# Kernel optimization log

Measured on AMD Instinct MI355X. Metric: run time of the kernel, lower is better.

Reference implementation:

```python
import jax, jax.numpy as jnp
import numpy as np

N = 100000
E = 640000
D = 128
L = 3
B = 128
OUT = 10


def setup_inputs() -> dict:
    key = jax.random.key(0)
    ks = jax.random.split(key, 8)
    x = jax.random.normal(ks[0], (N, D), dtype=jnp.float32)
    edge_index = jax.random.randint(ks[1], (2, E), 0, N, dtype=jnp.int64)
    batch = jnp.sort(jax.random.randint(ks[2], (N,), 0, B, dtype=jnp.int64))
    # per-layer GCNConv weights (in==hidden==D so they stack) and biases
    Ws = jax.random.normal(ks[3], (L, D, D), dtype=jnp.float32) / np.sqrt(D)
    bs = jnp.zeros((L, D), dtype=jnp.float32)
    # MLP head: single Linear(hidden -> out), norm=None
    W_mlp = jax.random.normal(ks[4], (D, OUT), dtype=jnp.float32) / np.sqrt(D)
    b_mlp = jnp.zeros((OUT,), dtype=jnp.float32)
    return {"x": x, "edge_index": edge_index, "batch": batch,
            "Ws": Ws, "bs": bs, "W_mlp": W_mlp, "b_mlp": b_mlp}


def reference(x, edge_index, batch, Ws, bs, W_mlp, b_mlp):
    n = x.shape[0]
    # --- GCN normalization (PyG gcn_norm with self-loops, edge_weight=1) ---
    loop = jnp.arange(n, dtype=edge_index.dtype)
    src = jnp.concatenate([edge_index[0], loop])  # message sources (x_j)
    dst = jnp.concatenate([edge_index[1], loop])  # aggregation targets
    deg = jax.ops.segment_sum(jnp.ones_like(dst, dtype=x.dtype), dst, num_segments=n)
    dinv = jnp.where(deg > 0, jax.lax.rsqrt(jnp.maximum(deg, 1.0)), 0.0)
    norm = dinv[src] * dinv[dst]  # [E+N]

    def gcn_conv(h, W, b):
        hw = h @ W  # [N, D] dense transform
        msg = hw[src] * norm[:, None]  # gather + scale [E+N, D]
        agg = jax.ops.segment_sum(msg, dst, num_segments=n)  # scatter-add
        return agg + b

    h = x
    for l in range(Ws.shape[0]):
        h = jax.nn.relu(gcn_conv(h, Ws[l], bs[l]))

    # global add pool over graphs
    pooled = jax.ops.segment_sum(h, batch, num_segments=B)  # [B, D]
    # MLP head (single linear, no norm/act)
    return pooled @ W_mlp + b_mlp
```

## Files before the change

### kernel.cpp

```cpp
#include <hip/hip_runtime.h>
#include <hip/hip_bf16.h>

#define N_NODES 100000
#define N_EDGES 640000
#define DIM 128
#define N_LAYERS 3
#define N_GRAPHS 128
#define N_OUT 10
#define SCAN_BLK 1024
#define N_SCAN_BLKS ((N_NODES + SCAN_BLK - 1) / SCAN_BLK)
#define PCHUNK 128
#define NXCD 8
#define RNODES (N_NODES / NXCD)
#define R_EST 98304
#define BE 1000
#define RK 40
#define GEMM_GRID 512

typedef _Float16 h4 __attribute__((ext_vector_type(4)));
typedef _Float16 h2 __attribute__((ext_vector_type(2)));
typedef _Float16 h8 __attribute__((ext_vector_type(8)));
typedef float f32x4 __attribute__((ext_vector_type(4)));


__global__ __launch_bounds__(256) void bucket_edges(const int* __restrict__ ei,
                                                    int* __restrict__ rangeCur,
                                                    int2* __restrict__ staging) {
    __shared__ int hist[NXCD];
    __shared__ int base[NXCD];
    const int e0 = blockIdx.x * BE;
    if (threadIdx.x < NXCD) hist[threadIdx.x] = 0;
    __syncthreads();

    int s[4], d[4], r[4];
    #pragma unroll
    for (int k = 0; k < 4; ++k) {
        int e = e0 + threadIdx.x + k * 256;
        if (e < e0 + BE) {
            s[k] = ei[e];
            d[k] = ei[N_EDGES + e];
            r[k] = d[k] / RNODES;
            atomicAdd(&hist[r[k]], 1);
        } else r[k] = -1;
    }
    __syncthreads();
    if (threadIdx.x < NXCD) base[threadIdx.x] = atomicAdd(&rangeCur[threadIdx.x], hist[threadIdx.x]);
    __syncthreads();
    if (threadIdx.x < NXCD) hist[threadIdx.x] = 0;
    __syncthreads();

    #pragma unroll
    for (int k = 0; k < 4; ++k) {
        if (r[k] >= 0) {
            int idx = base[r[k]] + atomicAdd(&hist[r[k]], 1);
            staging[(size_t)r[k] * R_EST + idx] = make_int2(s[k], d[k]);
        }
    }
}


__global__ __launch_bounds__(256) void hist_pinned(const int2* __restrict__ staging,
                                                   const int* __restrict__ rangeCur,
                                                   int* __restrict__ cnt) {
    const int g = blockIdx.x & (NXCD - 1);
    const int b = blockIdx.x >> 3;
    const int n = rangeCur[g];
    const int2* st = staging + (size_t)g * R_EST;
    for (int j = b * 256 + threadIdx.x; j < n; j += RK * 256)
        atomicAdd(&cnt[st[j].y], 1);
}


__global__ void scan1(const int* __restrict__ cnt, int* __restrict__ off, int* __restrict__ bsum,
                      float* __restrict__ dinv) {
    __shared__ int tmp[256];
    int base = blockIdx.x * SCAN_BLK + threadIdx.x * 4;
    int c[4];
    #pragma unroll
    for (int k = 0; k < 4; ++k) c[k] = (base + k < N_NODES) ? cnt[base + k] : 0;
    #pragma unroll
    for (int k = 0; k < 4; ++k)
        if (base + k < N_NODES) dinv[base + k] = rsqrtf((float)(c[k] + 1));
    int tot = c[0] + c[1] + c[2] + c[3];
    tmp[threadIdx.x] = tot;
    __syncthreads();
    int val = tot;
    for (int d = 1; d < 256; d <<= 1) {
        int add = (threadIdx.x >= d) ? tmp[threadIdx.x - d] : 0;
        __syncthreads();
        val += add;
        tmp[threadIdx.x] = val;
        __syncthreads();
    }
    int ex = val - tot;
    int e1 = ex + c[0], e2 = e1 + c[1], e3 = e2 + c[2];
    if (base + 0 < N_NODES) off[base + 0] = ex;
    if (base + 1 < N_NODES) off[base + 1] = e1;
    if (base + 2 < N_NODES) off[base + 2] = e2;
    if (base + 3 < N_NODES) off[base + 3] = e3;
    if (threadIdx.x == 255) bsum[blockIdx.x] = val;
}

__global__ void scan2(int* __restrict__ bsum) {
    __shared__ int tmp[128];
    int t = threadIdx.x;
    int v = (t < N_SCAN_BLKS) ? bsum[t] : 0;
    int own = v;
    tmp[t] = v;
    __syncthreads();
    for (int d = 1; d < 128; d <<= 1) {
        int add = (t >= d) ? tmp[t - d] : 0;
        __syncthreads();
        v += add;
        tmp[t] = v;
        __syncthreads();
    }
    if (t < N_SCAN_BLKS) bsum[t] = v - own;
}

__global__ void scan3(int* __restrict__ off, const int* __restrict__ bsum) {
    int i = blockIdx.x * blockDim.x + threadIdx.x;
    if (i < N_NODES) off[i] += bsum[i / SCAN_BLK];
    if (i == 0) off[N_NODES] = N_EDGES;
}


__global__ __launch_bounds__(256) void fill_pinned(const int2* __restrict__ staging,
                                                   const int* __restrict__ rangeCur,
                                                   const int* __restrict__ off,
                                                   int* __restrict__ cursor,
                                                   int* __restrict__ csr_src) {
    const int g = blockIdx.x & (NXCD - 1);
    const int b = blockIdx.x >> 3;
    const int n = rangeCur[g];
    const int2* st = staging + (size_t)g * R_EST;
    for (int j = b * 256 + threadIdx.x; j < n; j += RK * 256) {
        int2 sd = st[j];
        int pos = off[sd.y] + atomicAdd(&cursor[sd.y], 1);
        csr_src[pos] = sd.x;
    }
}


__global__ void wt_prep(const float* __restrict__ Ws, _Float16* __restrict__ wt) {
    int t = blockIdx.x * blockDim.x + threadIdx.x;
    if (t >= N_LAYERS * DIM * 32) return;
    int u = t & 31;
    int n = (t >> 5) & 127;
    int l = t >> 12;
    const float* W = Ws + (size_t)l * DIM * DIM;
    int k0 = u * 4;
    h4 v;
    v.x = (_Float16)W[(k0 + 0) * DIM + n];
    v.y = (_Float16)W[(k0 + 1) * DIM + n];
    v.z = (_Float16)W[(k0 + 2) * DIM + n];
    v.w = (_Float16)W[(k0 + 3) * DIM + n];
    int du = u ^ (n & 31);
    ((h4*)wt)[(size_t)l * 4096 + n * 32 + du] = v;
}


__device__ __forceinline__ h4 loadfrag(const _Float16* p) { return *(const h4*)p; }
__device__ __forceinline__ h4 loadfrag(const float* p) {
    float4 f = *(const float4*)p;
    h4 v; v.x = (_Float16)f.x; v.y = (_Float16)f.y; v.z = (_Float16)f.z; v.w = (_Float16)f.w;
    return v;
}

template<typename TIN>
__global__ __launch_bounds__(256) void gemm_mfma(const TIN* __restrict__ in,
                                                 const _Float16* __restrict__ wt,
                                                 const float* __restrict__ dinv,
                                                 _Float16* __restrict__ out) {
    __shared__ h4 Wl[4096];
    {
        const float4* src = (const float4*)wt;
        float4* dst = (float4*)Wl;
        #pragma unroll
        for (int i = 0; i < 8; ++i) dst[threadIdx.x + i * 256] = src[threadIdx.x + i * 256];
    }
    __syncthreads();

    const int wave = threadIdx.x >> 6;
    const int lane = threadIdx.x & 63;
    const int row = lane & 15;
    const int g   = lane >> 4;
    const int STEP = GEMM_GRID * 64;

    int c0 = blockIdx.x * 64;
    h4 bf[8];
    float di = 0.f;
    bool valid = false;
    {
        int m0 = c0 + wave * 16;
        if (c0 < N_NODES && m0 < N_NODES) {
            valid = true;
            const TIN* ar = in + (size_t)(m0 + row) * DIM;
            di = dinv[m0 + row];
            #pragma unroll
            for (int kc = 0; kc < 8; ++kc) bf[kc] = loadfrag(ar + kc * 16 + g * 4);
        }
    }

    for (; c0 < N_NODES; c0 += STEP) {
        const int c1 = c0 + STEP;
        h4 bf2[8];
        float di2 = 0.f;
        bool valid2 = false;
        if (c1 < N_NODES) {
            int m1 = c1 + wave * 16;
            if (m1 < N_NODES) {
                valid2 = true;
                const TIN* ar2 = in + (size_t)(m1 + row) * DIM;
                di2 = dinv[m1 + row];
                #pragma unroll
                for (int kc = 0; kc < 8; ++kc) bf2[kc] = loadfrag(ar2 + kc * 16 + g * 4);
            }
        }

        if (valid) {
            f32x4 acc[8] = {};
            #pragma unroll
            for (int kc = 0; kc < 8; ++kc) {
                const int u = kc * 4 + g;
                #pragma unroll
                for (int nb = 0; nb < 8; ++nb) {
                    const int n = nb * 16 + row;
                    const h4 afrag = Wl[n * 32 + (u ^ (n & 31))];
                    acc[nb] = __builtin_amdgcn_mfma_f32_16x16x16f16(afrag, bf[kc], acc[nb], 0, 0, 0);
                }
            }
            _Float16* orow = out + (size_t)(c0 + wave * 16 + row) * DIM;
            #pragma unroll
            for (int nb = 0; nb < 8; ++nb) {
                h4 v;
                v.x = (_Float16)(acc[nb].x * di); v.y = (_Float16)(acc[nb].y * di);
                v.z = (_Float16)(acc[nb].z * di); v.w = (_Float16)(acc[nb].w * di);
                ((h4*)orow)[nb * 4 + g] = v;
            }
        }

        #pragma unroll
        for (int kc = 0; kc < 8; ++kc) bf[kc] = bf2[kc];
        di = di2;
        valid = valid2;
    }
}


__global__ __launch_bounds__(256) void gather_agg(const _Float16* __restrict__ hw,
                                                  const float* __restrict__ dinv,
                                                  const int* __restrict__ off,
                                                  const int* __restrict__ csr_src,
                                                  const float* __restrict__ bias,
                                                  _Float16* __restrict__ hout) {
    const int i = (blockIdx.x * blockDim.x + threadIdx.x) >> 6;
    if (i >= N_NODES) return;
    const int lane = threadIdx.x & 63;
    const int grp    = lane >> 3;
    const int stream = grp & 3;
    const int half   = grp >> 2;
    const int sub    = lane & 7;
    const int idx8   = half * 8 + sub;
    const h8* hw8 = (const h8*)hw;

    const int beg = off[i], end = off[i + 1];
    h8 acc = {};

    if (stream == 3) acc = hw8[(size_t)i * 16 + idx8];

    int j = beg + stream;
    for (; j + 4 < end; j += 8) {
        int s0 = csr_src[j];
        int s1 = csr_src[j + 4];
        h8 v0 = hw8[(size_t)s0 * 16 + idx8];
        h8 v1 = hw8[(size_t)s1 * 16 + idx8];
        #pragma unroll
        for (int p = 0; p < 4; ++p) {
            ((h2*)&acc)[p] += ((h2*)&v0)[p];
            ((h2*)&acc)[p] += ((h2*)&v1)[p];
        }
    }
    for (; j < end; j += 4) {
        int s0 = csr_src[j];
        h8 v0 = hw8[(size_t)s0 * 16 + idx8];
        #pragma unroll
        for (int p = 0; p < 4; ++p) ((h2*)&acc)[p] += ((h2*)&v0)[p];
    }

    unsigned int* au = (unsigned int*)&acc;
    #pragma unroll
    for (int p = 0; p < 4; ++p) {
        unsigned int o = __shfl_xor(au[p], 8);
        h2 a = *(h2*)&au[p]; a += *(h2*)&o; au[p] = *(unsigned int*)&a;
        o = __shfl_xor(au[p], 16);
        h2 b = *(h2*)&au[p]; b += *(h2*)&o; au[p] = *(unsigned int*)&b;
    }

    if (stream == 0) {
        const float di = dinv[i];
        const float4 b0 = *(const float4*)&bias[half * 64 + sub * 8];
        const float4 b1 = *(const float4*)&bias[half * 64 + sub * 8 + 4];
        h8 v;
        v[0] = (_Float16)fmaxf((float)acc[0] * di + b0.x, 0.0f);
        v[1] = (_Float16)fmaxf((float)acc[1] * di + b0.y, 0.0f);
        v[2] = (_Float16)fmaxf((float)acc[2] * di + b0.z, 0.0f);
        v[3] = (_Float16)fmaxf((float)acc[3] * di + b0.w, 0.0f);
        v[4] = (_Float16)fmaxf((float)acc[4] * di + b1.x, 0.0f);
        v[5] = (_Float16)fmaxf((float)acc[5] * di + b1.y, 0.0f);
        v[6] = (_Float16)fmaxf((float)acc[6] * di + b1.z, 0.0f);
        v[7] = (_Float16)fmaxf((float)acc[7] * di + b1.w, 0.0f);
        ((h8*)hout)[(size_t)i * 16 + idx8] = v;
    }
}


__global__ __launch_bounds__(256) void pool_chunk(const _Float16* __restrict__ h,
                                                  const int* __restrict__ batch,
                                                  float* __restrict__ pooled) {
    const int base = blockIdx.x * PCHUNK;
    const int t = threadIdx.x;
    const int lane4 = t & 31;
    const int rgrp = t >> 5;
    const h4* hp = (const h4*)h;

    float a0 = 0.f, a1 = 0.f, a2 = 0.f, a3 = 0.f;
    int cur = -1;
    const int rend = (base + PCHUNK < N_NODES) ? base + PCHUNK : N_NODES;
    for (int r = base + rgrp; r < rend; r += 8) {
        int b = batch[r];
        if (b != cur) {
            if (cur >= 0) {
                float* pp = &pooled[cur * DIM + lane4 * 4];
                atomicAdd(pp + 0, a0); atomicAdd(pp + 1, a1);
                atomicAdd(pp + 2, a2); atomicAdd(pp + 3, a3);
            }
            cur = b; a0 = a1 = a2 = a3 = 0.f;
        }
        h4 v = hp[(size_t)r * 32 + lane4];
        a0 += (float)v.x; a1 += (float)v.y; a2 += (float)v.z; a3 += (float)v.w;
    }
    if (cur >= 0) {
        float* pp = &pooled[cur * DIM + lane4 * 4];
        atomicAdd(pp + 0, a0); atomicAdd(pp + 1, a1);
        atomicAdd(pp + 2, a2); atomicAdd(pp + 3, a3);
    }
}


__global__ void mlp_head(const float* __restrict__ pooled, const float* __restrict__ Wm,
                         const float* __restrict__ bm, float* __restrict__ out) {
    int t = blockIdx.x * blockDim.x + threadIdx.x;
    if (t >= N_GRAPHS * N_OUT) return;
    int b = t / N_OUT;
    int o = t % N_OUT;
    float acc = bm[o];
    #pragma unroll 8
    for (int k = 0; k < DIM; ++k) acc += pooled[b * DIM + k] * Wm[k * N_OUT + o];
    out[t] = acc;
}


extern "C" void kernel_launch(void* const* d_in, const int* in_sizes, int n_in,
                              void* d_out, int out_size, void* d_ws, size_t ws_size,
                              hipStream_t stream) {
    const float* x     = (const float*)d_in[0];
    const int*   ei    = (const int*)d_in[1];
    const int*   batch = (const int*)d_in[2];
    const float* Ws    = (const float*)d_in[3];
    const float* bs    = (const float*)d_in[4];
    const float* Wm    = (const float*)d_in[5];
    const float* bm    = (const float*)d_in[6];
    float* out = (float*)d_out;

    char* p = (char*)d_ws;
    int*      cnt      = (int*)p;        p += N_NODES * 4;
    int*      cursor   = (int*)p;        p += N_NODES * 4;
    int*      rangeCur = (int*)p;        p += 16 * 4;
    float*    dinv     = (float*)p;      p += N_NODES * 4;
    int*      csr_off  = (int*)p;        p += (N_NODES + 16) * 4;
    int*      bsum     = (int*)p;        p += 128 * 4;
    _Float16* wt       = (_Float16*)p;   p += (size_t)N_LAYERS * DIM * DIM * 2;
    int*      csr_src  = (int*)p;        p += (size_t)N_EDGES * 4;
    int2*     staging  = (int2*)p;       p += (size_t)NXCD * R_EST * 8;
    _Float16* bufA     = (_Float16*)p;   p += (size_t)N_NODES * DIM * 2;
    _Float16* bufB     = (_Float16*)p;   p += (size_t)N_NODES * DIM * 2;
    float*    pooled   = (float*)p;      p += N_GRAPHS * DIM * 4;

    const int nnode_blk = (N_NODES + 255) / 256;

    hipMemsetAsync(cnt, 0, N_NODES * 8 + 16 * 4, stream);
    hipMemsetAsync(pooled, 0, N_GRAPHS * DIM * 4, stream);

    bucket_edges<<<N_EDGES / BE, 256, 0, stream>>>(ei, rangeCur, staging);
    wt_prep<<<(N_LAYERS * DIM * 32 + 255) / 256, 256, 0, stream>>>(Ws, wt);

    hist_pinned<<<NXCD * RK, 256, 0, stream>>>(staging, rangeCur, cnt);

    scan1<<<N_SCAN_BLKS, 256, 0, stream>>>(cnt, csr_off, bsum, dinv);
    scan2<<<1, 128, 0, stream>>>(bsum);
    scan3<<<nnode_blk, 256, 0, stream>>>(csr_off, bsum);

    fill_pinned<<<NXCD * RK, 256, 0, stream>>>(staging, rangeCur, csr_off, cursor, csr_src);

    const int gather_grid = (N_NODES * 64 + 255) / 256;
    for (int l = 0; l < N_LAYERS; ++l) {
        if (l == 0) gemm_mfma<float><<<GEMM_GRID, 256, 0, stream>>>(x, wt, dinv, bufA);
        else        gemm_mfma<_Float16><<<GEMM_GRID, 256, 0, stream>>>(bufB, wt + (size_t)l * DIM * DIM, dinv, bufA);
        gather_agg<<<gather_grid, 256, 0, stream>>>(bufA, dinv, csr_off, csr_src, bs + l * DIM, bufB);
    }

    pool_chunk<<<(N_NODES + PCHUNK - 1) / PCHUNK, 256, 0, stream>>>(bufB, batch, pooled);
    mlp_head<<<(N_GRAPHS * N_OUT + 255) / 256, 256, 0, stream>>>(pooled, Wm, bm, out);
}
```

Measured before the change: 286.1 us.

## Pack staged edges into 32 bits and keep GEMM weights in registers

Each staged edge is packed into one 32-bit word: 17 bits of source index plus the destination's offset within its range. This halves the staging traffic in bucket, hist and fill. The GEMM no longer stages the weight matrix in LDS. Each lane preloads its 64 MFMA A-fragments into registers from a pre-swizzled layout, under launch_bounds(256,2). This removes LDS reads and the block barrier, at the cost of high register pressure and possible spills. Bounds checks on partial tiles were also dropped, which relies on N_NODES being a multiple of 16.

```diff
diff --git a/kernel.cpp b/kernel.cpp
--- a/kernel.cpp
+++ b/kernel.cpp
@@ -16,6 +16,7 @@
 #define BE 1000
 #define RK 40
 #define GEMM_GRID 512
+#define SMASK 0x1FFFF
 
 typedef _Float16 h4 __attribute__((ext_vector_type(4)));
 typedef _Float16 h2 __attribute__((ext_vector_type(2)));
@@ -25,21 +26,22 @@
 
 __global__ __launch_bounds__(256) void bucket_edges(const int* __restrict__ ei,
                                                     int* __restrict__ rangeCur,
-                                                    int2* __restrict__ staging) {
+                                                    unsigned int* __restrict__ staging) {
     __shared__ int hist[NXCD];
     __shared__ int base[NXCD];
     const int e0 = blockIdx.x * BE;
     if (threadIdx.x < NXCD) hist[threadIdx.x] = 0;
     __syncthreads();
 
-    int s[4], d[4], r[4];
+    unsigned int pk[4]; int r[4];
     #pragma unroll
     for (int k = 0; k < 4; ++k) {
         int e = e0 + threadIdx.x + k * 256;
         if (e < e0 + BE) {
-            s[k] = ei[e];
-            d[k] = ei[N_EDGES + e];
-            r[k] = d[k] / RNODES;
+            int s = ei[e];
+            int d = ei[N_EDGES + e];
+            r[k] = d / RNODES;
+            pk[k] = (unsigned int)s | ((unsigned int)(d - r[k] * RNODES) << 17);
             atomicAdd(&hist[r[k]], 1);
         } else r[k] = -1;
     }
@@ -53,21 +55,22 @@
     for (int k = 0; k < 4; ++k) {
         if (r[k] >= 0) {
             int idx = base[r[k]] + atomicAdd(&hist[r[k]], 1);
-            staging[(size_t)r[k] * R_EST + idx] = make_int2(s[k], d[k]);
-        }
-    }
-}
-
-
-__global__ __launch_bounds__(256) void hist_pinned(const int2* __restrict__ staging,
+            staging[(size_t)r[k] * R_EST + idx] = pk[k];
+        }
+    }
+}
+
+
+__global__ __launch_bounds__(256) void hist_pinned(const unsigned int* __restrict__ staging,
                                                    const int* __restrict__ rangeCur,
                                                    int* __restrict__ cnt) {
     const int g = blockIdx.x & (NXCD - 1);
     const int b = blockIdx.x >> 3;
     const int n = rangeCur[g];
-    const int2* st = staging + (size_t)g * R_EST;
+    const unsigned int* st = staging + (size_t)g * R_EST;
+    const int dbase = g * RNODES;
     for (int j = b * 256 + threadIdx.x; j < n; j += RK * 256)
-        atomicAdd(&cnt[st[j].y], 1);
+        atomicAdd(&cnt[dbase + (st[j] >> 17)], 1);
 }
 
 
@@ -125,7 +128,7 @@
 }
 
 
-__global__ __launch_bounds__(256) void fill_pinned(const int2* __restrict__ staging,
+__global__ __launch_bounds__(256) void fill_pinned(const unsigned int* __restrict__ staging,
                                                    const int* __restrict__ rangeCur,
                                                    const int* __restrict__ off,
                                                    int* __restrict__ cursor,
@@ -133,30 +136,32 @@
     const int g = blockIdx.x & (NXCD - 1);
     const int b = blockIdx.x >> 3;
     const int n = rangeCur[g];
-    const int2* st = staging + (size_t)g * R_EST;
+    const unsigned int* st = staging + (size_t)g * R_EST;
+    const int dbase = g * RNODES;
     for (int j = b * 256 + threadIdx.x; j < n; j += RK * 256) {
-        int2 sd = st[j];
-        int pos = off[sd.y] + atomicAdd(&cursor[sd.y], 1);
-        csr_src[pos] = sd.x;
+        unsigned int v = st[j];
+        int d = dbase + (int)(v >> 17);
+        int pos = off[d] + atomicAdd(&cursor[d], 1);
+        csr_src[pos] = (int)(v & SMASK);
     }
 }
 
 
 __global__ void wt_prep(const float* __restrict__ Ws, _Float16* __restrict__ wt) {
     int t = blockIdx.x * blockDim.x + threadIdx.x;
-    if (t >= N_LAYERS * DIM * 32) return;
-    int u = t & 31;
-    int n = (t >> 5) & 127;
+    if (t >= N_LAYERS * 64 * 64) return;
+    int lane = t & 63;
+    int j = (t >> 6) & 63;
     int l = t >> 12;
     const float* W = Ws + (size_t)l * DIM * DIM;
-    int k0 = u * 4;
+    int n = (j >> 3) * 16 + (lane & 15);
+    int k0 = (j & 7) * 16 + (lane >> 4) * 4;
     h4 v;
     v.x = (_Float16)W[(k0 + 0) * DIM + n];
     v.y = (_Float16)W[(k0 + 1) * DIM + n];
     v.z = (_Float16)W[(k0 + 2) * DIM + n];
     v.w = (_Float16)W[(k0 + 3) * DIM + n];
-    int du = u ^ (n & 31);
-    ((h4*)wt)[(size_t)l * 4096 + n * 32 + du] = v;
+    ((h4*)wt)[(size_t)l * 4096 + j * 64 + lane] = v;
 }
 
 
@@ -168,33 +173,29 @@
 }
 
 template<typename TIN>
-__global__ __launch_bounds__(256) void gemm_mfma(const TIN* __restrict__ in,
-                                                 const _Float16* __restrict__ wt,
-                                                 const float* __restrict__ dinv,
-                                                 _Float16* __restrict__ out) {
-    __shared__ h4 Wl[4096];
-    {
-        const float4* src = (const float4*)wt;
-        float4* dst = (float4*)Wl;
-        #pragma unroll
-        for (int i = 0; i < 8; ++i) dst[threadIdx.x + i * 256] = src[threadIdx.x + i * 256];
-    }
-    __syncthreads();
-
+__global__ __launch_bounds__(256, 2) void gemm_mfma(const TIN* __restrict__ in,
+                                                    const _Float16* __restrict__ wt,
+                                                    const float* __restrict__ dinv,
+                                                    _Float16* __restrict__ out) {
     const int wave = threadIdx.x >> 6;
     const int lane = threadIdx.x & 63;
     const int row = lane & 15;
     const int g   = lane >> 4;
     const int STEP = GEMM_GRID * 64;
 
+    h4 w[64];
+    {
+        const h4* wsrc = (const h4*)wt + lane;
+        #pragma unroll
+        for (int j = 0; j < 64; ++j) w[j] = wsrc[j * 64];
+    }
+
     int c0 = blockIdx.x * 64;
     h4 bf[8];
     float di = 0.f;
-    bool valid = false;
     {
         int m0 = c0 + wave * 16;
-        if (c0 < N_NODES && m0 < N_NODES) {
-            valid = true;
+        if (c0 < N_NODES) {
             const TIN* ar = in + (size_t)(m0 + row) * DIM;
             di = dinv[m0 + row];
             #pragma unroll
@@ -206,28 +207,21 @@
         const int c1 = c0 + STEP;
         h4 bf2[8];
         float di2 = 0.f;
-        bool valid2 = false;
         if (c1 < N_NODES) {
             int m1 = c1 + wave * 16;
-            if (m1 < N_NODES) {
-                valid2 = true;
-                const TIN* ar2 = in + (size_t)(m1 + row) * DIM;
-                di2 = dinv[m1 + row];
-                #pragma unroll
-                for (int kc = 0; kc < 8; ++kc) bf2[kc] = loadfrag(ar2 + kc * 16 + g * 4);
-            }
-        }
-
-        if (valid) {
+            const TIN* ar2 = in + (size_t)(m1 + row) * DIM;
+            di2 = dinv[m1 + row];
+            #pragma unroll
+            for (int kc = 0; kc < 8; ++kc) bf2[kc] = loadfrag(ar2 + kc * 16 + g * 4);
+        }
+
+        {
             f32x4 acc[8] = {};
             #pragma unroll
             for (int kc = 0; kc < 8; ++kc) {
-                const int u = kc * 4 + g;
                 #pragma unroll
                 for (int nb = 0; nb < 8; ++nb) {
-                    const int n = nb * 16 + row;
-                    const h4 afrag = Wl[n * 32 + (u ^ (n & 31))];
-                    acc[nb] = __builtin_amdgcn_mfma_f32_16x16x16f16(afrag, bf[kc], acc[nb], 0, 0, 0);
+                    acc[nb] = __builtin_amdgcn_mfma_f32_16x16x16f16(w[nb * 8 + kc], bf[kc], acc[nb], 0, 0, 0);
                 }
             }
             _Float16* orow = out + (size_t)(c0 + wave * 16 + row) * DIM;
@@ -243,7 +237,6 @@
         #pragma unroll
         for (int kc = 0; kc < 8; ++kc) bf[kc] = bf2[kc];
         di = di2;
-        valid = valid2;
     }
 }
 
@@ -374,18 +367,18 @@
     float* out = (float*)d_out;
 
     char* p = (char*)d_ws;
-    int*      cnt      = (int*)p;        p += N_NODES * 4;
-    int*      cursor   = (int*)p;        p += N_NODES * 4;
-    int*      rangeCur = (int*)p;        p += 16 * 4;
-    float*    dinv     = (float*)p;      p += N_NODES * 4;
-    int*      csr_off  = (int*)p;        p += (N_NODES + 16) * 4;
-    int*      bsum     = (int*)p;        p += 128 * 4;
-    _Float16* wt       = (_Float16*)p;   p += (size_t)N_LAYERS * DIM * DIM * 2;
-    int*      csr_src  = (int*)p;        p += (size_t)N_EDGES * 4;
-    int2*     staging  = (int2*)p;       p += (size_t)NXCD * R_EST * 8;
-    _Float16* bufA     = (_Float16*)p;   p += (size_t)N_NODES * DIM * 2;
-    _Float16* bufB     = (_Float16*)p;   p += (size_t)N_NODES * DIM * 2;
-    float*    pooled   = (float*)p;      p += N_GRAPHS * DIM * 4;
+    int*          cnt      = (int*)p;          p += N_NODES * 4;
+    int*          cursor   = (int*)p;          p += N_NODES * 4;
+    int*          rangeCur = (int*)p;          p += 16 * 4;
+    float*        dinv     = (float*)p;        p += N_NODES * 4;
+    int*          csr_off  = (int*)p;          p += (N_NODES + 16) * 4;
+    int*          bsum     = (int*)p;          p += 128 * 4;
+    _Float16*     wt       = (_Float16*)p;     p += (size_t)N_LAYERS * DIM * DIM * 2;
+    int*          csr_src  = (int*)p;          p += (size_t)N_EDGES * 4;
+    unsigned int* staging  = (unsigned int*)p; p += (size_t)NXCD * R_EST * 4;
+    _Float16*     bufA     = (_Float16*)p;     p += (size_t)N_NODES * DIM * 2;
+    _Float16*     bufB     = (_Float16*)p;     p += (size_t)N_NODES * DIM * 2;
+    float*        pooled   = (float*)p;        p += N_GRAPHS * DIM * 4;
 
     const int nnode_blk = (N_NODES + 255) / 256;
 
@@ -393,7 +386,7 @@
     hipMemsetAsync(pooled, 0, N_GRAPHS * DIM * 4, stream);
 
     bucket_edges<<<N_EDGES / BE, 256, 0, stream>>>(ei, rangeCur, staging);
-    wt_prep<<<(N_LAYERS * DIM * 32 + 255) / 256, 256, 0, stream>>>(Ws, wt);
+    wt_prep<<<(N_LAYERS * 64 * 64 + 255) / 256, 256, 0, stream>>>(Ws, wt);
 
     hist_pinned<<<NXCD * RK, 256, 0, stream>>>(staging, rangeCur, cnt);
 
```

After: 294.4 us. +2.9%, slower.
